# Performance work log

Hardware: AMD Instinct MI355X
Metric: run time of the kernel (lower is better)

The kernel has to match this reference:

```python
import jax, jax.numpy as jnp
import numpy as np

N, C, K, KEIG, B, NG, H = 32768, 128, 5, 128, 64, 512, 4
E = 524288
EPS = 1e-5


def setup_inputs() -> dict:
    key = jax.random.key(0)
    ks = iter(jax.random.split(key, 40))
    def nrm(shape, scale):
        return jax.random.normal(next(ks), shape, jnp.float32) * scale
    s = 1.0 / np.sqrt(C)
    return dict(
        x=nrm((N, C), 1.0),
        U=nrm((N, KEIG), 1.0 / np.sqrt(N)),
        Lambda=jax.random.uniform(next(ks), (KEIG,), jnp.float32, 0.0, 2.0),
        lambda_max=jnp.full((1,), 2.0, jnp.float32),
        w_spa1=nrm((C, C), s), b_spa1=jnp.zeros((C,), jnp.float32),
        w_spa2=nrm((C, C), s), b_spa2=jnp.zeros((C,), jnp.float32),
        w_spe1=nrm((C, C), s), b_spe1=jnp.zeros((C,), jnp.float32),
        w_spe2=nrm((C, C), s), b_spe2=jnp.zeros((C,), jnp.float32),
        cheb_w=nrm((K, C, C), s), cheb_b=jnp.zeros((C,), jnp.float32),
        gamma=jnp.ones((1,), jnp.float32),
        w_proj=nrm((C, C), s),
        w_qkv=nrm((C, 3 * C), s), b_qkv=jnp.zeros((3 * C,), jnp.float32),
        w_out=nrm((C, C), s), b_out=jnp.zeros((C,), jnp.float32),
        mlp_w1=nrm((C, 2 * C), s), mlp_b1=jnp.zeros((2 * C,), jnp.float32),
        mlp_w2=nrm((2 * C, C), 1.0 / np.sqrt(2 * C)), mlp_b2=jnp.zeros((C,), jnp.float32),
        bn1_w=jnp.ones((C,), jnp.float32), bn1_b=jnp.zeros((C,), jnp.float32),
        bn2_w=jnp.ones((C,), jnp.float32), bn2_b=jnp.zeros((C,), jnp.float32),
        bn3_w=jnp.ones((C,), jnp.float32), bn3_b=jnp.zeros((C,), jnp.float32),
        edge_index=jax.random.randint(next(ks), (2, E), 0, N, jnp.int64) if jax.config.jax_enable_x64 else jax.random.randint(next(ks), (2, E), 0, N, jnp.int32),
        batch=jnp.repeat(jnp.arange(B), NG),  # 64 graphs of 512 nodes each
    )


def _mlp2(h, w1, b1, w2, b2):
    return jnp.maximum(h @ w1 + b1, 0.0) @ w2 + b2


def _bn(h, w, b):
    # train-mode BatchNorm1d over node dim (biased variance), GPSConv default norm
    mu = h.mean(0)
    var = jnp.mean((h - mu) ** 2, 0)
    return (h - mu) * jax.lax.rsqrt(var + EPS) * w + b


def _cheb(x, src, dst, lam, Ws, bias):
    # L_hat = (2/lambda_max) * (I - D^{-1/2} A D^{-1/2}) - I ; sym normalization
    deg = jax.ops.segment_sum(jnp.ones_like(src, x.dtype), src, num_segments=N)
    dis = jnp.where(deg > 0, 1.0 / jnp.sqrt(deg), 0.0)
    w = dis[src] * dis[dst]  # [E]
    scale = 2.0 / lam
    def lhat(v):
        agg = jax.ops.segment_sum(w[:, None] * v[src], dst, num_segments=N)
        return (scale - 1.0) * v - scale * agg
    Tx0 = x
    out = Tx0 @ Ws[0]
    Tx1 = lhat(Tx0)
    out = out + Tx1 @ Ws[1]
    for k in range(2, K):
        Tx2 = 2.0 * lhat(Tx1) - Tx0
        out = out + Tx2 @ Ws[k]
        Tx0, Tx1 = Tx1, Tx2
    return out + bias


def _mha(xd, w_qkv, b_qkv, w_out, b_out):
    Bq, n, _ = xd.shape
    dh = C // H
    qkv = xd @ w_qkv + b_qkv  # [B,n,3C]
    q, k, v = jnp.split(qkv, 3, axis=-1)
    heads = lambda t: t.reshape(Bq, n, H, dh).transpose(0, 2, 1, 3)
    q, k, v = heads(q), heads(k), heads(v)
    a = jax.nn.softmax(jnp.einsum('bhqd,bhkd->bhqk', q, k) / np.sqrt(dh), axis=-1)
    o = jnp.einsum('bhqk,bhkd->bhqd', a, v).transpose(0, 2, 1, 3).reshape(Bq, n, C)
    return o @ w_out + b_out


def reference(x, U, Lambda, lambda_max,
              w_spa1, b_spa1, w_spa2, b_spa2,
              w_spe1, b_spe1, w_spe2, b_spe2,
              cheb_w, cheb_b, gamma, w_proj,
              w_qkv, b_qkv, w_out, b_out,
              mlp_w1, mlp_b1, mlp_w2, mlp_b2,
              bn1_w, bn1_b, bn2_w, bn2_b, bn3_w, bn3_b,
              edge_index, batch):
    src, dst = edge_index[0], edge_index[1]
    lam = lambda_max[0]
    # ---- SpectralLocalNN (GPSConv local conv branch) ----
    x_sp = _mlp2(x, w_spa1, b_spa1, w_spa2, b_spa2)
    out_local = _cheb(x_sp, src, dst, lam, cheb_w, cheb_b)
    x_spec = _mlp2(x, w_spe1, b_spe1, w_spe2, b_spe2)
    h_proj = x_spec @ w_proj
    s_lam = jnp.exp(-gamma[0] * Lambda ** 2)  # [k_eig]
    out_spectral = U @ (s_lam[:, None] * (U.T @ h_proj))
    h1 = _bn(out_local + out_spectral + x, bn1_w, bn1_b)
    # ---- global attention branch (equal-size graphs -> dense reshape) ----
    xd = x.reshape(B, NG, C)
    h2 = _mha(xd, w_qkv, b_qkv, w_out, b_out).reshape(N, C)
    h2 = _bn(h2 + x, bn2_w, bn2_b)
    # ---- combine + MLP ----
    out = h1 + h2
    out = out + _mlp2(out, mlp_w1, mlp_b1, mlp_w2, mlp_b2)
    return _bn(out, bn3_w, bn3_b)
```

## Files before the change

### kernel.cpp

```cpp
#include <hip/hip_runtime.h>

typedef short bf16x8 __attribute__((ext_vector_type(8)));
typedef short bf16x4 __attribute__((ext_vector_type(4)));
typedef float f32x4 __attribute__((ext_vector_type(4)));

#define DEVI __device__ __forceinline__

constexpr int N   = 32768;
constexpr int C   = 128;
constexpr int E   = 524288;
constexpr float EPSV = 1e-5f;
constexpr int UT_BLOCKS = 256;
constexpr int HB  = 64;
constexpr int EPB = E / HB;

DEVI float bf2f(ushort u){ return __uint_as_float(((uint)u) << 16); }
DEVI ushort f2bf(float f){
  uint u = __float_as_uint(f);
  return (ushort)((u + 0x7fffu + ((u >> 16) & 1u)) >> 16);
}
DEVI float sane(float v){ if (!(v == v)) return 0.f; return fminf(fmaxf(v, -1e30f), 1e30f); }
DEVI bool mode_fp32(const uint* lmraw){ return (lmraw[0] & 0xffffu) == 0u; }

constexpr int CSZ[28] = {128,1,16384,128,16384,128,16384,128,16384,128,81920,128,
                         1,16384,49152,384,16384,128,32768,256,32768,128,
                         128,128,128,128,128,128};
constexpr int COF[28] = {0,128,192,16576,16704,33088,33216,49600,49728,66112,
                         66240,148160,148288,148352,164736,213888,214272,230656,
                         230784,263552,263808,296576,296704,296832,296960,297088,
                         297216,297344};
constexpr int CAN_SMALL_TOTAL = 297472;

struct CvtArgs { const void* src[28]; };

__global__ __launch_bounds__(256) void convert_small(CvtArgs a, ushort* __restrict__ can,
                                                     const uint* __restrict__ lmraw)
{
  bool f32 = mode_fp32(lmraw);
  int idx = blockIdx.x * 256 + threadIdx.x;
  #pragma unroll 1
  for (int s = 0; s < 28; s++) {
    if (idx < CSZ[s]) {
      ushort v = f32 ? f2bf(((const float*)a.src[s])[idx])
                     : ((const ushort*)a.src[s])[idx];
      can[COF[s] + idx] = v;
      return;
    }
    idx -= CSZ[s];
  }
}

__global__ __launch_bounds__(256) void convert_big(const void* __restrict__ xs,
    const void* __restrict__ Us, ushort* __restrict__ canx, ushort* __restrict__ canu,
    const uint* __restrict__ lmraw)
{
  bool f32 = mode_fp32(lmraw);
  size_t e = ((size_t)blockIdx.x * 256 + threadIdx.x) * 4;
  bool isU = e >= (size_t)N * C;
  size_t off = isU ? e - (size_t)N * C : e;
  const void* src = isU ? Us : xs;
  ushort* dst = isU ? canu : canx;
  ushort4 o;
  if (f32) {
    float4 v = *(const float4*)((const float*)src + off);
    o.x = f2bf(v.x); o.y = f2bf(v.y); o.z = f2bf(v.z); o.w = f2bf(v.w);
  } else {
    o = *(const ushort4*)((const ushort*)src + off);
  }
  *(ushort4*)(dst + off) = o;
}

__global__ __launch_bounds__(1024) void hist_lds(const int* __restrict__ ei,
    int* __restrict__ cei, ushort* __restrict__ part)
{
  __shared__ uint hist[N / 2];
  int t = threadIdx.x;
  int b = blockIdx.x;
  bool i64 = ((ei[1] | ei[3] | ei[5] | ei[7]) == 0);
  size_t j0 = (size_t)b * EPB;
  #pragma unroll
  for (int i = t; i < N / 2; i += 1024) hist[i] = 0u;
  __syncthreads();
  for (int k = t; k < EPB; k += 1024) {
    size_t j = j0 + k;
    int v = (i64 ? ei[2 * j] : ei[j]) & (N - 1);
    cei[j] = v;
    atomicAdd(&hist[v >> 1], 1u << ((v & 1) * 16));
  }
  __syncthreads();
  uint* po = (uint*)(part + (size_t)b * N);
  for (int i = t; i < N / 2; i += 1024) po[i] = hist[i];
}

__global__ __launch_bounds__(256) void reduce_cnt(const ushort* __restrict__ part,
    int* __restrict__ cdt, float* __restrict__ dis)
{
  int d = blockIdx.x * 256 + threadIdx.x;
  int s = 0, tt = 0;
  #pragma unroll 8
  for (int b = 0; b < HB; b++) s  += part[(size_t)b * N + d];
  #pragma unroll 8
  for (int b = 0; b < HB; b++) tt += part[(size_t)(HB + b) * N + d];
  cdt[d] = tt;
  dis[d] = s > 0 ? rsqrtf((float)s) : 0.f;
}

__global__ __launch_bounds__(1024) void scan_kernel(const int* __restrict__ cnt,
                                                    int* __restrict__ row_ptr)
{
  __shared__ int sums[1024];
  int t = threadIdx.x;
  int loc[32]; int s = 0;
  int base = t * 32;
  #pragma unroll
  for (int i = 0; i < 32; i++) { loc[i] = s; s += cnt[base + i]; }
  sums[t] = s;
  __syncthreads();
  for (int off = 1; off < 1024; off <<= 1) {
    int v = (t >= off) ? sums[t - off] : 0;
    __syncthreads();
    sums[t] += v;
    __syncthreads();
  }
  int pre = (t == 0) ? 0 : sums[t - 1];
  #pragma unroll
  for (int i = 0; i < 32; i++) row_ptr[base + i] = pre + loc[i];
}

__global__ __launch_bounds__(256) void off_kernel(const int* __restrict__ rp,
    const ushort* __restrict__ part, int* __restrict__ off2)
{
  int d = blockIdx.x * 256 + threadIdx.x;
  int run = rp[d];
  #pragma unroll 8
  for (int b = 0; b < HB; b++) {
    off2[(size_t)b * N + d] = run;
    run += part[(size_t)(HB + b) * N + d];
  }
}

__global__ __launch_bounds__(1024) void edge_scatter(const int* __restrict__ cei,
    const int* __restrict__ off2, const float* __restrict__ dis,
    int2* __restrict__ ep)
{
  __shared__ int base[N];
  int t = threadIdx.x;
  int b = blockIdx.x;
  for (int i = t; i < N; i += 1024) base[i] = off2[(size_t)b * N + i];
  __syncthreads();
  size_t e0 = (size_t)b * EPB;
  for (int k = t; k < EPB; k += 1024) {
    size_t e = e0 + k;
    int s = cei[e], d = cei[e + E];
    int slot = atomicAdd(&base[d], 1);
    int2 v; v.x = s; v.y = __float_as_int(dis[s] * dis[d]);
    ep[slot] = v;
  }
}

constexpr int WT_SPA1 = 0;
constexpr int WT_SPA2 = 16384;
constexpr int WT_SPE1 = 32768;
constexpr int WT_SPE2 = 49152;
constexpr int WT_PROJ = 65536;
constexpr int WT_CHEB = 81920;
constexpr int WT_QKV  = 163840;
constexpr int WT_WOUT = 212992;
constexpr int WT_MLP1 = 229376;
constexpr int WT_MLP2 = 262144;
constexpr int WT_TOTAL = 294912;

__global__ __launch_bounds__(256) void zero_kernel(int* __restrict__ p, int n)
{
  int i = blockIdx.x * 256 + threadIdx.x;
  if (i < n) p[i] = 0;
}

__global__ __launch_bounds__(256) void transpose_weights(
    const ushort* __restrict__ spa1, const ushort* __restrict__ spa2,
    const ushort* __restrict__ spe1, const ushort* __restrict__ spe2,
    const ushort* __restrict__ proj, const ushort* __restrict__ cheb,
    const ushort* __restrict__ qkv,  const ushort* __restrict__ wout,
    const ushort* __restrict__ mlp1, const ushort* __restrict__ mlp2,
    ushort* __restrict__ wt)
{
  int i = blockIdx.x * 256 + threadIdx.x;
  if (i < 81920) {
    int m = i >> 14, r = i & 16383; int k = r >> 7, n = r & 127;
    const ushort* src = m==0?spa1 : m==1?spa2 : m==2?spe1 : m==3?spe2 : proj;
    wt[m*16384 + n*128 + k] = src[r];
  } else if (i < 163840) {
    int j = i - 81920; int m = j >> 14, r = j & 16383; int k = r >> 7, n = r & 127;
    wt[WT_CHEB + n*640 + m*128 + k] = cheb[j];
  } else if (i < 212992) {
    int j = i - 163840; int k = j / 384, n = j % 384;
    wt[WT_QKV + n*128 + k] = qkv[j];
  } else if (i < 229376) {
    int j = i - 212992; int k = j >> 7, n = j & 127;
    wt[WT_WOUT + n*128 + k] = wout[j];
  } else if (i < 262144) {
    int j = i - 229376; int k = j >> 8, n = j & 255;
    wt[WT_MLP1 + n*128 + k] = mlp1[j];
  } else if (i < WT_TOTAL) {
    int j = i - 262144; int k = j >> 7, n = j & 127;
    wt[WT_MLP2 + n*256 + k] = mlp2[j];
  }
}

template<int K, int COLS, bool RELU, int OMODE, bool BIAS, bool RES, int ASTR, int OSTR>
__global__ __launch_bounds__(256) void gemm_lds(
    const ushort* __restrict__ A, const ushort* __restrict__ WT,
    const ushort* __restrict__ bias, const ushort* __restrict__ res,
    void* __restrict__ outp)
{
  constexpr int NSEG = COLS / 128;
  constexpr int NKC = K / 128;
  constexpr int BP = 136;
  __shared__ ushort Bs[128 * BP];
  int tid = threadIdx.x;
  int lane = tid & 63, wave = tid >> 6;
  int quad = lane >> 4, l16 = lane & 15;
  int seg = (NSEG > 1) ? (blockIdx.x % NSEG) : 0;
  int rb  = (NSEG > 1) ? (blockIdx.x / NSEG) : blockIdx.x;
  int row0 = rb * 64 + wave * 16;
  const ushort* wseg = WT + (size_t)(seg * 128) * K;

  f32x4 acc[8];
  #pragma unroll
  for (int nt = 0; nt < 8; nt++) acc[nt] = (f32x4){0.f, 0.f, 0.f, 0.f};

  for (int kc = 0; kc < NKC; kc++) {
    if (kc) __syncthreads();
    #pragma unroll
    for (int i = tid; i < 2048; i += 256) {
      int col = i >> 4, ko = (i & 15) * 8;
      *(bf16x8*)&Bs[col * BP + ko] =
          *(const bf16x8*)(wseg + (size_t)col * K + kc * 128 + ko);
    }
    __syncthreads();
    bf16x8 a[4];
    const ushort* ap = A + (size_t)(row0 + l16) * ASTR + kc * 128 + quad * 8;
    #pragma unroll
    for (int kk = 0; kk < 4; kk++) a[kk] = *(const bf16x8*)(ap + kk * 32);
    #pragma unroll
    for (int kk = 0; kk < 4; kk++) {
      #pragma unroll
      for (int nt = 0; nt < 8; nt++) {
        bf16x8 b = *(const bf16x8*)(&Bs[(nt * 16 + l16) * BP + kk * 32 + quad * 8]);
        acc[nt] = __builtin_amdgcn_mfma_f32_16x16x32_bf16(a[kk], b, acc[nt], 0, 0, 0);
      }
    }
  }

  #pragma unroll
  for (int nt = 0; nt < 8; nt++) {
    int col = seg * 128 + nt * 16 + l16;
    float bv = 0.f;
    if (BIAS) bv = bf2f(bias[col]);
    #pragma unroll
    for (int r = 0; r < 4; r++) {
      int row = row0 + quad * 4 + r;
      size_t oi = (size_t)row * OSTR + col;
      float v = acc[nt][r] + bv;
      if (RES) v += bf2f(res[(size_t)row * COLS + col]);
      if (RELU) v = fmaxf(v, 0.f);
      if (OMODE == 0)      ((ushort*)outp)[oi] = f2bf(v);
      else if (OMODE == 1) ((float*)outp)[oi] = v;
      else                 ((float*)outp)[oi] += v;
    }
  }
}

__global__ __launch_bounds__(256) void spmm_cheb(
    const int* __restrict__ row_ptr, const int2* __restrict__ ep,
    const ushort* __restrict__ v,
    const ushort* __restrict__ txprev, ushort* __restrict__ txout,
    const ushort* __restrict__ lambda_max, int first, int str)
{
  int wave = threadIdx.x >> 6, lane = threadIdx.x & 63;
  int sub = lane >> 4, l16 = lane & 15;
  int d = blockIdx.x * 4 + wave;
  float lm = bf2f(lambda_max[0]);
  float scale = 2.f / lm;
  if (!(scale == scale) || fabsf(scale) > 1e6f) scale = 1.f;
  int beg = row_ptr[d];
  int end = (d == N - 1) ? E : row_ptr[d + 1];
  float acc[8] = {0.f,0.f,0.f,0.f,0.f,0.f,0.f,0.f};
  for (int jb = beg; jb < end; jb += 4) {
    int j = jb + sub;
    bool ok = j < end;
    int2 e2 = ep[ok ? j : beg];
    int s = e2.x & (N - 1);
    float w = ok ? __int_as_float(e2.y) : 0.f;
    bf16x8 vv = *(const bf16x8*)(v + (size_t)s * str + l16 * 8);
    #pragma unroll
    for (int i = 0; i < 8; i++) acc[i] += w * bf2f((ushort)vv[i]);
  }
  #pragma unroll
  for (int i = 0; i < 8; i++) {
    acc[i] += __shfl_xor(acc[i], 16);
    acc[i] += __shfl_xor(acc[i], 32);
  }
  if (sub == 0) {
    bf16x8 vd = *(const bf16x8*)(v + (size_t)d * str + l16 * 8);
    bf16x8 tp;
    if (!first) tp = *(const bf16x8*)(txprev + (size_t)d * str + l16 * 8);
    bf16x8 ov;
    #pragma unroll
    for (int i = 0; i < 8; i++) {
      float r = (scale - 1.f) * bf2f((ushort)vd[i]) - scale * acc[i];
      if (!first) r = 2.f * r - bf2f((ushort)tp[i]);
      ov[i] = (short)f2bf(r);
    }
    *(bf16x8*)(txout + (size_t)d * str + l16 * 8) = ov;
  }
}

__global__ __launch_bounds__(256) void ut_mfma(const ushort* __restrict__ U,
    const ushort* __restrict__ hp, float* __restrict__ parts)
{
  constexpr int RP = 40;
  __shared__ ushort Ut[128 * RP];
  __shared__ ushort Ht[128 * RP];
  int t = threadIdx.x;
  int lane = t & 63, wave = t >> 6;
  int quad = lane >> 4, l16 = lane & 15;

  f32x4 acc[2][8];
  #pragma unroll
  for (int a = 0; a < 2; a++)
    #pragma unroll
    for (int ct = 0; ct < 8; ct++) acc[a][ct] = (f32x4){0.f, 0.f, 0.f, 0.f};

  for (int ch = 0; ch < 4; ch++) {
    int n0 = blockIdx.x * 128 + ch * 32;
    __syncthreads();
    for (int i = t; i < 2048; i += 256) {
      int r2 = i >> 7, c = i & 127;
      uint u0 = U [(size_t)(n0 + r2 * 2) * 128 + c];
      uint u1 = U [(size_t)(n0 + r2 * 2 + 1) * 128 + c];
      *(uint*)&Ut[c * RP + r2 * 2] = (u0 & 0xffffu) | (u1 << 16);
      uint h0 = hp[(size_t)(n0 + r2 * 2) * 128 + c];
      uint h1 = hp[(size_t)(n0 + r2 * 2 + 1) * 128 + c];
      *(uint*)&Ht[c * RP + r2 * 2] = (h0 & 0xffffu) | (h1 << 16);
    }
    __syncthreads();
    bf16x8 bfr[8];
    #pragma unroll
    for (int ct = 0; ct < 8; ct++)
      bfr[ct] = *(const bf16x8*)(&Ht[(ct * 16 + l16) * RP + quad * 8]);
    #pragma unroll
    for (int a = 0; a < 2; a++) {
      int kt = wave * 2 + a;
      bf16x8 af = *(const bf16x8*)(&Ut[(kt * 16 + l16) * RP + quad * 8]);
      #pragma unroll
      for (int ct = 0; ct < 8; ct++)
        acc[a][ct] = __builtin_amdgcn_mfma_f32_16x16x32_bf16(af, bfr[ct], acc[a][ct], 0, 0, 0);
    }
  }

  float* po = parts + (size_t)blockIdx.x * 16384;
  #pragma unroll
  for (int a = 0; a < 2; a++) {
    int kt = wave * 2 + a;
    #pragma unroll
    for (int ct = 0; ct < 8; ct++)
      #pragma unroll
      for (int r = 0; r < 4; r++)
        po[(kt * 16 + quad * 4 + r) * 128 + ct * 16 + l16] = acc[a][ct][r];
  }
}

__global__ __launch_bounds__(256) void reduce_mt(const float* __restrict__ parts,
    const ushort* __restrict__ Lambda, const ushort* __restrict__ gamma,
    ushort* __restrict__ MT)
{
  int e = blockIdx.x * 256 + threadIdx.x;
  int keig = e >> 7, c = e & 127;
  float s = 0.f;
  for (int p = 0; p < UT_BLOCKS; p++) s += parts[(size_t)p * 16384 + e];
  float g = bf2f(gamma[0]);
  float lam = bf2f(Lambda[keig]);
  float sl = __expf(-g * lam * lam);
  MT[c * 128 + keig] = f2bf(sl * s);
}

__global__ __launch_bounds__(256) void bn_stats(const float* __restrict__ h,
                                                float* __restrict__ stats)
{
  int c = threadIdx.x & 127, half = threadIdx.x >> 7;
  int r0 = blockIdx.x * 128 + half;
  float s = 0.f, s2 = 0.f;
  for (int i = 0; i < 64; i++) {
    float v = sane(h[(size_t)(r0 + i * 2) * 128 + c]);
    s += v; s2 += v * v;
  }
  atomicAdd(&stats[c], s);
  atomicAdd(&stats[128 + c], s2);
}

__global__ __launch_bounds__(256) void bn_apply(const float* __restrict__ h,
    const float* __restrict__ st, const ushort* __restrict__ gw,
    const ushort* __restrict__ gb, const ushort* __restrict__ add,
    void* __restrict__ out, const uint* __restrict__ lmraw, int final_out)
{
  size_t e = ((size_t)blockIdx.x * 256 + threadIdx.x) * 4;
  int c0 = (int)(e & 127);
  float4 hv = *(const float4*)(h + e);
  float xv[4] = {sane(hv.x), sane(hv.y), sane(hv.z), sane(hv.w)};
  float addv[4] = {0.f, 0.f, 0.f, 0.f};
  if (add) {
    ushort4 av = *(const ushort4*)(add + e);
    addv[0] = bf2f(av.x); addv[1] = bf2f(av.y);
    addv[2] = bf2f(av.z); addv[3] = bf2f(av.w);
  }
  float r[4];
  #pragma unroll
  for (int j = 0; j < 4; j++) {
    int c = c0 + j;
    float mu = st[c] * (1.f / 32768.f);
    float var = fmaxf(st[128 + c] * (1.f / 32768.f) - mu * mu, 0.f);
    r[j] = (xv[j] - mu) * rsqrtf(var + EPSV) * bf2f(gw[c]) + bf2f(gb[c]) + addv[j];
  }
  if (final_out && mode_fp32(lmraw)) {
    float4 o4; o4.x = r[0]; o4.y = r[1]; o4.z = r[2]; o4.w = r[3];
    *(float4*)((float*)out + e) = o4;
  } else {
    ushort4 o;
    o.x = f2bf(r[0]); o.y = f2bf(r[1]); o.z = f2bf(r[2]); o.w = f2bf(r[3]);
    *(ushort4*)((ushort*)out + e) = o;
  }
}

__global__ __launch_bounds__(256) void attn_mfma(const ushort* __restrict__ qkv,
                                                 ushort* __restrict__ attn)
{
  constexpr int VP = 520;
  __shared__ ushort Vt[32 * VP];
  int b = blockIdx.x;
  int g = b >> 3, hh = (b >> 1) & 3, half = b & 1;
  int lane = threadIdx.x & 63, wave = threadIdx.x >> 6;
  int quad = lane >> 4, l16 = lane & 15;
  const ushort* base = qkv + (size_t)g * 512 * 384;

  for (int i = threadIdx.x; i < 512 * 8; i += 256) {
    int key = i >> 3, d4 = (i & 7) * 4;
    ushort4 v4 = *(const ushort4*)(base + key * 384 + 256 + hh * 32 + d4);
    Vt[(d4 + 0) * VP + key] = v4.x;
    Vt[(d4 + 1) * VP + key] = v4.y;
    Vt[(d4 + 2) * VP + key] = v4.z;
    Vt[(d4 + 3) * VP + key] = v4.w;
  }
  __syncthreads();

  int q0 = half * 256 + wave * 64;
  bf16x8 qf[4];
  #pragma unroll
  for (int i = 0; i < 4; i++)
    qf[i] = *(const bf16x8*)(base + (size_t)(q0 + i * 16 + l16) * 384 + hh * 32 + quad * 8);

  f32x4 O[2][4];
  #pragma unroll
  for (int dt = 0; dt < 2; dt++)
    #pragma unroll
    for (int i = 0; i < 4; i++) O[dt][i] = (f32x4){0.f, 0.f, 0.f, 0.f};
  float lsum[4] = {0.f, 0.f, 0.f, 0.f};
  const float SC = 0.17677669529663687f;

  for (int kt = 0; kt < 32; kt++) {
    bf16x8 kf = *(const bf16x8*)(base + (size_t)(kt * 16 + l16) * 384 + 128 + hh * 32 + quad * 8);
    bf16x8 pf[4];
    #pragma unroll
    for (int i = 0; i < 4; i++) {
      f32x4 s = __builtin_amdgcn_mfma_f32_16x16x32_bf16(kf, qf[i], (f32x4){0.f,0.f,0.f,0.f}, 0, 0, 0);
      float p0 = __expf(fminf(s[0] * SC, 60.f));
      float p1 = __expf(fminf(s[1] * SC, 60.f));
      float p2 = __expf(fminf(s[2] * SC, 60.f));
      float p3 = __expf(fminf(s[3] * SC, 60.f));
      lsum[i] += p0 + p1 + p2 + p3;
      pf[i] = (bf16x8){(short)f2bf(p0), (short)f2bf(p1), (short)f2bf(p2), (short)f2bf(p3), 0, 0, 0, 0};
    }
    #pragma unroll
    for (int dt = 0; dt < 2; dt++) {
      bf16x4 v4 = *(const bf16x4*)(&Vt[(dt * 16 + l16) * VP + kt * 16 + quad * 4]);
      bf16x8 vf = (bf16x8){v4[0], v4[1], v4[2], v4[3], 0, 0, 0, 0};
      #pragma unroll
      for (int i = 0; i < 4; i++)
        O[dt][i] = __builtin_amdgcn_mfma_f32_16x16x32_bf16(vf, pf[i], O[dt][i], 0, 0, 0);
    }
  }

  #pragma unroll
  for (int i = 0; i < 4; i++) {
    float l = lsum[i];
    l += __shfl_xor(l, 16);
    l += __shfl_xor(l, 32);
    lsum[i] = 1.f / l;
  }

  #pragma unroll
  for (int i = 0; i < 4; i++) {
    size_t node = (size_t)g * 512 + q0 + i * 16 + l16;
    #pragma unroll
    for (int dt = 0; dt < 2; dt++) {
      ushort4 o;
      o.x = f2bf(O[dt][i][0] * lsum[i]);
      o.y = f2bf(O[dt][i][1] * lsum[i]);
      o.z = f2bf(O[dt][i][2] * lsum[i]);
      o.w = f2bf(O[dt][i][3] * lsum[i]);
      *(ushort4*)(attn + node * 128 + hh * 32 + dt * 16 + quad * 4) = o;
    }
  }
}

constexpr size_t KB = 1024;
constexpr size_t MB = 1048576;
constexpr size_t OFF_WT    = 0;
constexpr size_t OFF_CDT   = 576 * KB;
constexpr size_t OFF_RP    = 704 * KB;
constexpr size_t OFF_DIS   = 832 * KB;
constexpr size_t OFF_MT    = 960 * KB;
constexpr size_t OFF_STATS = 1024 * KB;
constexpr size_t OFF_CEI   = 6  * MB;
constexpr size_t OFF_EP    = 10 * MB;
constexpr size_t OFF_CANX  = 14 * MB;
constexpr size_t OFF_CANU  = 22 * MB;
constexpr size_t OFF_CANS  = 30 * MB;
constexpr size_t OFF_F1    = 31 * MB;
constexpr size_t OFF_SPEC  = 31 * MB;
constexpr size_t OFF_HPROJ = 39 * MB;
constexpr size_t OFF_TBIG  = 47 * MB;
constexpr size_t OFF_PARTH = OFF_TBIG;
constexpr size_t OFF_OFF2  = OFF_TBIG + 8 * MB;
constexpr size_t OFF_PARTS = 87 * MB;

extern "C" void kernel_launch(void* const* d_in, const int* in_sizes, int n_in,
                              void* d_out, int out_size, void* d_ws, size_t ws_size,
                              hipStream_t stream) {
  (void)in_sizes; (void)n_in; (void)out_size; (void)ws_size;
  const uint* lmraw = (const uint*)d_in[3];
  const int*  ei    = (const int*)d_in[30];

  char* W = (char*)d_ws;
  ushort* wt    = (ushort*)(W + OFF_WT);
  int*    cdt   = (int*)(W + OFF_CDT);
  int*    rp    = (int*)(W + OFF_RP);
  float*  dis   = (float*)(W + OFF_DIS);
  ushort* MT    = (ushort*)(W + OFF_MT);
  float*  stats = (float*)(W + OFF_STATS);
  int*    cei   = (int*)(W + OFF_CEI);
  int2*   ep    = (int2*)(W + OFF_EP);
  ushort* part  = (ushort*)(W + OFF_PARTH);
  int*    off2  = (int*)(W + OFF_OFF2);
  ushort* canx  = (ushort*)(W + OFF_CANX);
  ushort* canu  = (ushort*)(W + OFF_CANU);
  ushort* cs    = (ushort*)(W + OFF_CANS);
  float*  F1    = (float*)(W + OFF_F1);
  ushort* spec  = (ushort*)(W + OFF_SPEC);
  ushort* tmpA  = (ushort*)(W + OFF_HPROJ);
  ushort* hproj = (ushort*)(W + OFF_HPROJ);
  ushort* Tbig  = (ushort*)(W + OFF_TBIG);
  ushort* qkvb  = (ushort*)(W + OFF_TBIG);
  ushort* mlph  = (ushort*)(W + OFF_TBIG);
  float*  parts = (float*)(W + OFF_PARTS);
  ushort* attnb = (ushort*)(W + OFF_PARTS);
  ushort* h1    = (ushort*)(W + OFF_CANU);
  ushort* comb  = (ushort*)(W + OFF_CANX);

  const ushort* cLambda = cs + COF[0];
  const ushort* cLmx    = cs + COF[1];
  const ushort* cSpa1   = cs + COF[2];
  const ushort* cBspa1  = cs + COF[3];
  const ushort* cSpa2   = cs + COF[4];
  const ushort* cBspa2  = cs + COF[5];
  const ushort* cSpe1   = cs + COF[6];
  const ushort* cBspe1  = cs + COF[7];
  const ushort* cSpe2   = cs + COF[8];
  const ushort* cBspe2  = cs + COF[9];
  const ushort* cCheb   = cs + COF[10];
  const ushort* cChebB  = cs + COF[11];
  const ushort* cGam    = cs + COF[12];
  const ushort* cProj   = cs + COF[13];
  const ushort* cQkv    = cs + COF[14];
  const ushort* cBqkv   = cs + COF[15];
  const ushort* cWout   = cs + COF[16];
  const ushort* cBout   = cs + COF[17];
  const ushort* cMw1    = cs + COF[18];
  const ushort* cMb1    = cs + COF[19];
  const ushort* cMw2    = cs + COF[20];
  const ushort* cMb2    = cs + COF[21];
  const ushort* cBn1w   = cs + COF[22];
  const ushort* cBn1b   = cs + COF[23];
  const ushort* cBn2w   = cs + COF[24];
  const ushort* cBn2b   = cs + COF[25];
  const ushort* cBn3w   = cs + COF[26];
  const ushort* cBn3b   = cs + COF[27];

  const ushort* NUL = nullptr;

  zero_kernel<<<3, 256, 0, stream>>>((int*)(W + OFF_STATS), 768);

  CvtArgs ca;
  ca.src[0]  = d_in[2];  ca.src[1]  = d_in[3];  ca.src[2]  = d_in[4];
  ca.src[3]  = d_in[5];  ca.src[4]  = d_in[6];  ca.src[5]  = d_in[7];
  ca.src[6]  = d_in[8];  ca.src[7]  = d_in[9];  ca.src[8]  = d_in[10];
  ca.src[9]  = d_in[11]; ca.src[10] = d_in[12]; ca.src[11] = d_in[13];
  ca.src[12] = d_in[14]; ca.src[13] = d_in[15]; ca.src[14] = d_in[16];
  ca.src[15] = d_in[17]; ca.src[16] = d_in[18]; ca.src[17] = d_in[19];
  ca.src[18] = d_in[20]; ca.src[19] = d_in[21]; ca.src[20] = d_in[22];
  ca.src[21] = d_in[23]; ca.src[22] = d_in[24]; ca.src[23] = d_in[25];
  ca.src[24] = d_in[26]; ca.src[25] = d_in[27]; ca.src[26] = d_in[28];
  ca.src[27] = d_in[29];
  convert_small<<<(CAN_SMALL_TOTAL + 255) / 256, 256, 0, stream>>>(ca, cs, lmraw);
  convert_big<<<(2 * N * C / 4) / 256, 256, 0, stream>>>(d_in[0], d_in[1], canx, canu, lmraw);

  transpose_weights<<<1152, 256, 0, stream>>>(cSpa1, cSpa2, cSpe1, cSpe2,
      cProj, cCheb, cQkv, cWout, cMw1, cMw2, wt);

  hist_lds<<<2 * HB, 1024, 0, stream>>>(ei, cei, part);
  reduce_cnt<<<N / 256, 256, 0, stream>>>(part, cdt, dis);
  scan_kernel<<<1, 1024, 0, stream>>>(cdt, rp);
  off_kernel<<<N / 256, 256, 0, stream>>>(rp, part, off2);
  edge_scatter<<<HB, 1024, 0, stream>>>(cei, off2, dis, ep);

  dim3 g1(512), g2(1024), g3(1536), bb(256);
  gemm_lds<128,128,true ,0,true ,false,128,128><<<g1, bb, 0, stream>>>(canx, wt + WT_SPA1, cBspa1, NUL, tmpA);
  gemm_lds<128,128,false,0,true ,false,128,640><<<g1, bb, 0, stream>>>(tmpA, wt + WT_SPA2, cBspa2, NUL, Tbig);
  gemm_lds<128,128,true ,0,true ,false,128,128><<<g1, bb, 0, stream>>>(canx, wt + WT_SPE1, cBspe1, NUL, tmpA);
  gemm_lds<128,128,false,0,true ,false,128,128><<<g1, bb, 0, stream>>>(tmpA, wt + WT_SPE2, cBspe2, NUL, spec);
  gemm_lds<128,128,false,0,false,false,128,128><<<g1, bb, 0, stream>>>(spec, wt + WT_PROJ, NUL,    NUL, hproj);

  ut_mfma<<<UT_BLOCKS, 256, 0, stream>>>(canu, hproj, parts);
  reduce_mt<<<64, 256, 0, stream>>>(parts, cLambda, cGam, MT);

  spmm_cheb<<<N / 4, 256, 0, stream>>>(rp, ep, Tbig,       NUL,        Tbig + 128, cLmx, 1, 640);
  spmm_cheb<<<N / 4, 256, 0, stream>>>(rp, ep, Tbig + 128, Tbig,       Tbig + 256, cLmx, 0, 640);
  spmm_cheb<<<N / 4, 256, 0, stream>>>(rp, ep, Tbig + 256, Tbig + 128, Tbig + 384, cLmx, 0, 640);
  spmm_cheb<<<N / 4, 256, 0, stream>>>(rp, ep, Tbig + 384, Tbig + 256, Tbig + 512, cLmx, 0, 640);
  gemm_lds<640,128,false,1,true ,false,640,128><<<g1, bb, 0, stream>>>(Tbig, wt + WT_CHEB, cChebB, NUL, F1);

  gemm_lds<128,128,false,2,false,true ,128,128><<<g1, bb, 0, stream>>>(canu, MT, NUL, canx, F1);
  bn_stats<<<256, 256, 0, stream>>>(F1, stats);
  bn_apply<<<(N * C) / 1024, 256, 0, stream>>>(F1, stats, cBn1w, cBn1b, NUL, h1, lmraw, 0);

  gemm_lds<128,384,false,0,true ,false,128,384><<<g3, bb, 0, stream>>>(canx, wt + WT_QKV, cBqkv, NUL, qkvb);
  attn_mfma<<<512, 256, 0, stream>>>(qkvb, attnb);
  gemm_lds<128,128,false,1,true ,true ,128,128><<<g1, bb, 0, stream>>>(attnb, wt + WT_WOUT, cBout, canx, F1);
  bn_stats<<<256, 256, 0, stream>>>(F1, stats + 256);
  bn_apply<<<(N * C) / 1024, 256, 0, stream>>>(F1, stats + 256, cBn2w, cBn2b, h1, comb, lmraw, 0);

  gemm_lds<128,256,true ,0,true ,false,128,256><<<g2, bb, 0, stream>>>(comb, wt + WT_MLP1, cMb1, NUL, mlph);
  gemm_lds<256,128,false,1,true ,true ,256,128><<<g1, bb, 0, stream>>>(mlph, wt + WT_MLP2, cMb2, comb, F1);
  bn_stats<<<256, 256, 0, stream>>>(F1, stats + 512);
  bn_apply<<<(N * C) / 1024, 256, 0, stream>>>(F1, stats + 512, cBn3w, cBn3b, NUL, d_out, lmraw, 1);
}
```

Measured before the change: 552.1 us.

## Stage K in LDS and use full-depth MFMA for P·V in attention kernel

The attention kernel now copies the per-head K slice into padded shared memory instead of reading it from global memory on every key tile. It processes 32 keys per iteration so the P·V MFMA uses its full 32-deep K dimension rather than half-zero operands, halving the PV MFMA count. Softmax exponentials switch to exp2 with a prescaled constant, and bf16 packing uses the hardware v_cvt_pk_bf16_f32 instruction. The V transpose stores paired keys as 32-bit LDS writes. The cost is more LDS use per block, which may lower occupancy, and packed conversion rounding may differ slightly from the manual round-to-nearest-even.

```diff
diff --git a/kernel.cpp b/kernel.cpp
--- a/kernel.cpp
+++ b/kernel.cpp
@@ -18,6 +18,11 @@
 DEVI ushort f2bf(float f){
   uint u = __float_as_uint(f);
   return (ushort)((u + 0x7fffu + ((u >> 16) & 1u)) >> 16);
+}
+DEVI uint cvtpk(float lo, float hi){
+  uint r;
+  asm("v_cvt_pk_bf16_f32 %0, %1, %2" : "=v"(r) : "v"(lo), "v"(hi));
+  return r;
 }
 DEVI float sane(float v){ if (!(v == v)) return 0.f; return fminf(fmaxf(v, -1e30f), 1e30f); }
 DEVI bool mode_fp32(const uint* lmraw){ return (lmraw[0] & 0xffffu) == 0u; }
@@ -435,7 +440,9 @@
 __global__ __launch_bounds__(256) void attn_mfma(const ushort* __restrict__ qkv,
                                                  ushort* __restrict__ attn)
 {
-  constexpr int VP = 520;
+  constexpr int VP = 516;
+  constexpr int KP = 40;
+  __shared__ ushort Kt[512 * KP];
   __shared__ ushort Vt[32 * VP];
   int b = blockIdx.x;
   int g = b >> 3, hh = (b >> 1) & 3, half = b & 1;
@@ -443,13 +450,20 @@
   int quad = lane >> 4, l16 = lane & 15;
   const ushort* base = qkv + (size_t)g * 512 * 384;
 
-  for (int i = threadIdx.x; i < 512 * 8; i += 256) {
-    int key = i >> 3, d4 = (i & 7) * 4;
-    ushort4 v4 = *(const ushort4*)(base + key * 384 + 256 + hh * 32 + d4);
-    Vt[(d4 + 0) * VP + key] = v4.x;
-    Vt[(d4 + 1) * VP + key] = v4.y;
-    Vt[(d4 + 2) * VP + key] = v4.z;
-    Vt[(d4 + 3) * VP + key] = v4.w;
+  for (int i = threadIdx.x; i < 512 * 4; i += 256) {
+    int key = i >> 2, c8 = (i & 3) * 8;
+    *(bf16x8*)&Kt[key * KP + c8] =
+        *(const bf16x8*)(base + (size_t)key * 384 + 128 + hh * 32 + c8);
+  }
+  for (int i = threadIdx.x; i < 256 * 8; i += 256) {
+    int kp = i >> 3, d4 = (i & 7) * 4;
+    const ushort* va = base + (size_t)(2 * kp) * 384 + 256 + hh * 32 + d4;
+    ushort4 a = *(const ushort4*)va;
+    ushort4 c = *(const ushort4*)(va + 384);
+    *(uint*)&Vt[(d4 + 0) * VP + 2 * kp] = (uint)a.x | ((uint)c.x << 16);
+    *(uint*)&Vt[(d4 + 1) * VP + 2 * kp] = (uint)a.y | ((uint)c.y << 16);
+    *(uint*)&Vt[(d4 + 2) * VP + 2 * kp] = (uint)a.z | ((uint)c.z << 16);
+    *(uint*)&Vt[(d4 + 3) * VP + 2 * kp] = (uint)a.w | ((uint)c.w << 16);
   }
   __syncthreads();
 
@@ -465,28 +479,41 @@
     #pragma unroll
     for (int i = 0; i < 4; i++) O[dt][i] = (f32x4){0.f, 0.f, 0.f, 0.f};
   float lsum[4] = {0.f, 0.f, 0.f, 0.f};
-  const float SC = 0.17677669529663687f;
-
-  for (int kt = 0; kt < 32; kt++) {
-    bf16x8 kf = *(const bf16x8*)(base + (size_t)(kt * 16 + l16) * 384 + 128 + hh * 32 + quad * 8);
-    bf16x8 pf[4];
+  const float SC2 = 0.17677669529663687f * 1.4426950408889634f;
+
+  union PU { uint u[4]; bf16x8 v; };
+  union VU { uint2 a[2]; bf16x8 v; };
+
+  for (int kt2 = 0; kt2 < 16; kt2++) {
+    int k0 = kt2 * 32;
+    bf16x8 kfA = *(const bf16x8*)&Kt[(k0 + l16) * KP + quad * 8];
+    bf16x8 kfB = *(const bf16x8*)&Kt[(k0 + 16 + l16) * KP + quad * 8];
+    PU pw[4];
     #pragma unroll
     for (int i = 0; i < 4; i++) {
-      f32x4 s = __builtin_amdgcn_mfma_f32_16x16x32_bf16(kf, qf[i], (f32x4){0.f,0.f,0.f,0.f}, 0, 0, 0);
-      float p0 = __expf(fminf(s[0] * SC, 60.f));
-      float p1 = __expf(fminf(s[1] * SC, 60.f));
-      float p2 = __expf(fminf(s[2] * SC, 60.f));
-      float p3 = __expf(fminf(s[3] * SC, 60.f));
-      lsum[i] += p0 + p1 + p2 + p3;
-      pf[i] = (bf16x8){(short)f2bf(p0), (short)f2bf(p1), (short)f2bf(p2), (short)f2bf(p3), 0, 0, 0, 0};
+      f32x4 sA = __builtin_amdgcn_mfma_f32_16x16x32_bf16(kfA, qf[i], (f32x4){0.f,0.f,0.f,0.f}, 0, 0, 0);
+      f32x4 sB = __builtin_amdgcn_mfma_f32_16x16x32_bf16(kfB, qf[i], (f32x4){0.f,0.f,0.f,0.f}, 0, 0, 0);
+      float p0 = exp2f(fminf(sA[0] * SC2, 86.5f));
+      float p1 = exp2f(fminf(sA[1] * SC2, 86.5f));
+      float p2 = exp2f(fminf(sA[2] * SC2, 86.5f));
+      float p3 = exp2f(fminf(sA[3] * SC2, 86.5f));
+      float p4 = exp2f(fminf(sB[0] * SC2, 86.5f));
+      float p5 = exp2f(fminf(sB[1] * SC2, 86.5f));
+      float p6 = exp2f(fminf(sB[2] * SC2, 86.5f));
+      float p7 = exp2f(fminf(sB[3] * SC2, 86.5f));
+      lsum[i] += ((p0 + p1) + (p2 + p3)) + ((p4 + p5) + (p6 + p7));
+      pw[i].u[0] = cvtpk(p0, p1); pw[i].u[1] = cvtpk(p2, p3);
+      pw[i].u[2] = cvtpk(p4, p5); pw[i].u[3] = cvtpk(p6, p7);
     }
     #pragma unroll
     for (int dt = 0; dt < 2; dt++) {
-      bf16x4 v4 = *(const bf16x4*)(&Vt[(dt * 16 + l16) * VP + kt * 16 + quad * 4]);
-      bf16x8 vf = (bf16x8){v4[0], v4[1], v4[2], v4[3], 0, 0, 0, 0};
+      int drow = (dt * 16 + l16) * VP;
+      VU vu;
+      vu.a[0] = *(const uint2*)&Vt[drow + k0 + quad * 4];
+      vu.a[1] = *(const uint2*)&Vt[drow + k0 + 16 + quad * 4];
       #pragma unroll
       for (int i = 0; i < 4; i++)
-        O[dt][i] = __builtin_amdgcn_mfma_f32_16x16x32_bf16(vf, pf[i], O[dt][i], 0, 0, 0);
+        O[dt][i] = __builtin_amdgcn_mfma_f32_16x16x32_bf16(vu.v, pw[i].v, O[dt][i], 0, 0, 0);
     }
   }
 
@@ -503,12 +530,10 @@
     size_t node = (size_t)g * 512 + q0 + i * 16 + l16;
     #pragma unroll
     for (int dt = 0; dt < 2; dt++) {
-      ushort4 o;
-      o.x = f2bf(O[dt][i][0] * lsum[i]);
-      o.y = f2bf(O[dt][i][1] * lsum[i]);
-      o.z = f2bf(O[dt][i][2] * lsum[i]);
-      o.w = f2bf(O[dt][i][3] * lsum[i]);
-      *(ushort4*)(attn + node * 128 + hh * 32 + dt * 16 + quad * 4) = o;
+      uint2 o;
+      o.x = cvtpk(O[dt][i][0] * lsum[i], O[dt][i][1] * lsum[i]);
+      o.y = cvtpk(O[dt][i][2] * lsum[i], O[dt][i][3] * lsum[i]);
+      *(uint2*)(attn + node * 128 + hh * 32 + dt * 16 + quad * 4) = o;
     }
   }
 }
```

After: 547.6 us. Within noise of the previous version (-0.8%).
